# Optimization experiments

Measured on AMD Instinct MI355X. Metric: run time of the kernel, lower is better.

## Reference

```python
import jax, jax.numpy as jnp
import numpy as np

B, I, H = 128, 512, 512


def setup_inputs() -> dict:
    key = jax.random.key(0)
    ks = jax.random.split(key, 6)
    std = float(1.0 / np.sqrt(H))
    return {
        "x": jax.random.normal(ks[0], (B, I), jnp.float32),
        "h_prev": jax.random.normal(ks[1], (B, H), jnp.float32),
        "C_prev": jax.random.normal(ks[2], (B, H, H), jnp.float32),
        "m_prev": jnp.zeros((B, H), jnp.float32),
        "n_prev": jax.random.normal(ks[3], (B, H), jnp.float32),
        "W": jax.random.uniform(ks[4], (6 * H, I), jnp.float32, -std, std),
        "b": jax.random.uniform(ks[5], (6 * H,), jnp.float32, -std, std),
    }


def reference(x, h_prev, C_prev, m_prev, n_prev, W, b):
    # gates: [B, 6H] -> six [B, H] slices (input, forget, output, query, key, value)
    gates = x @ W.T + b
    ig, fg, og, q, k, v = jnp.split(gates, 6, axis=1)
    inv_sqrt_h = jnp.float32(1.0 / np.sqrt(H))
    k_t = inv_sqrt_h * k
    o_t = jax.nn.sigmoid(og)
    # log-domain stabilizer: log(exp(fg)) == fg, log(exp(ig)) == ig
    m_t = jnp.maximum(fg + m_prev, ig)
    i_t = jnp.exp(ig - m_t)
    f_t = jnp.exp(fg + m_prev - m_t)
    # matrix state update: broadcast-add of (i*v*k) column across last dim (as in source)
    C_t = f_t[:, :, None] * C_prev + (i_t * v * k_t)[:, :, None]  # [B,H,H]
    n_t = f_t * n_prev + i_t * k_t  # [B,H]
    # read-out: C_t @ q and n_t . q
    Cq = jnp.einsum("bij,bj->bi", C_t, q)  # [B,H]
    nq = jnp.einsum("bh,bh->b", n_t, q)  # [B]
    denom = jnp.maximum(jnp.abs(nq), jnp.float32(1e-6))
    h_t = o_t * (Cq / denom[:, None])
    return h_t, C_t, m_t, n_t
```

## Files before the change

kernel.cpp:

```cpp
#include <hip/hip_runtime.h>
#include <math.h>


#define B_SZ   128
#define H_DIM  512
#define I_DIM  512
#define G6     3072
#define BH     65536
#define CSZ    33554432

typedef float f32x4 __attribute__((ext_vector_type(4)));

__global__ __launch_bounds__(256) void gemm_gates(
    const float* __restrict__ x, const float* __restrict__ W,
    const float* __restrict__ bias, float* __restrict__ gates) {
  const int tid = threadIdx.x;
  const int c   = (blockIdx.x % 12) * 256 + tid;
  const int b0  = (blockIdx.x / 12) * 4;

  float acc[4];
#pragma unroll
  for (int j = 0; j < 4; ++j) acc[j] = 0.0f;

  const float4* wrow = reinterpret_cast<const float4*>(W + (size_t)c * I_DIM);
  const float4* x4   = reinterpret_cast<const float4*>(x);

#pragma unroll 4
  for (int t4 = 0; t4 < I_DIM / 4; ++t4) {
    const float4 wv = wrow[t4];
#pragma unroll
    for (int j = 0; j < 4; ++j) {
      const float4 xv = x4[(b0 + j) * (I_DIM / 4) + t4];
      acc[j] += xv.x * wv.x + xv.y * wv.y + xv.z * wv.z + xv.w * wv.w;
    }
  }
  const float bi = bias[c];
#pragma unroll
  for (int j = 0; j < 4; ++j)
    gates[(size_t)(b0 + j) * G6 + c] = acc[j] + bi;
}

__global__ __launch_bounds__(512) void gate_pointwise(
    const float* __restrict__ gates, const float* __restrict__ m_prev,
    const float* __restrict__ n_prev, float* __restrict__ out,
    float* __restrict__ f_arr, float* __restrict__ add_arr,
    float* __restrict__ o_arr, float* __restrict__ invden) {
  const int b = blockIdx.x;
  const int h = threadIdx.x;
  const float inv_sqrt_h = 0.044194173824159216f;

  const float* g = gates + (size_t)b * G6;
  float* out_m = out + BH + CSZ;
  float* out_n = out_m + BH;

  const float ig = g[h];
  const float fg = g[512 + h];
  const float og = g[1024 + h];
  const float q  = g[1536 + h];
  const float k  = g[2048 + h];
  const float v  = g[2560 + h];

  const int   idx = b * H_DIM + h;
  const float kt  = inv_sqrt_h * k;
  const float ot  = 1.0f / (1.0f + expf(-og));
  const float mp  = m_prev[idx];
  const float npv = n_prev[idx];
  const float mt  = fmaxf(fg + mp, ig);
  const float it  = expf(ig - mt);
  const float ft  = expf(fg + mp - mt);
  const float nt  = ft * npv + it * kt;

  out_m[idx]   = mt;
  out_n[idx]   = nt;
  f_arr[idx]   = ft;
  add_arr[idx] = it * v * kt;
  o_arr[idx]   = ot;

  __shared__ float red[512];
  red[h] = nt * q;
  __syncthreads();
#pragma unroll
  for (int s = 256; s > 0; s >>= 1) {
    if (h < s) red[h] += red[h + s];
    __syncthreads();
  }
  if (h == 0) {
    const float denom = fmaxf(fabsf(red[0]), 1e-6f);
    invden[b] = 1.0f / denom;
  }
}

__global__ __launch_bounds__(256) void update_C(
    const float* __restrict__ C_prev, const float* __restrict__ gates,
    const float* __restrict__ f_arr, const float* __restrict__ add_arr,
    const float* __restrict__ o_arr, const float* __restrict__ invden,
    float* __restrict__ out) {
  const int tid  = threadIdx.x;
  const int lane = tid & 63;
  const int w    = tid >> 6;
  const int r0   = blockIdx.x * 32;
  const int b    = r0 >> 9;

  const float4* q4 = reinterpret_cast<const float4*>(gates + (size_t)b * G6 + 1536);
  const float4 qa = q4[lane];
  const float4 qb = q4[lane + 64];
  const float inv_d = invden[b];

  float fv[8], av[8], hv[8];
#pragma unroll
  for (int it = 0; it < 8; ++it) {
    const int r = r0 + it * 4 + w;
    fv[it] = f_arr[r];
    av[it] = add_arr[r];
    hv[it] = o_arr[r];
  }

#pragma unroll
  for (int it = 0; it < 8; ++it) {
    const int r = r0 + it * 4 + w;
    const float f = fv[it];
    const float a = av[it];

    const f32x4* cp = reinterpret_cast<const f32x4*>(C_prev) + (size_t)r * 128;
    f32x4*       ct = reinterpret_cast<f32x4*>((float*)out + BH) + (size_t)r * 128;

    const f32x4 c0 = __builtin_nontemporal_load(cp + lane);
    const f32x4 c1 = __builtin_nontemporal_load(cp + lane + 64);

    f32x4 o0, o1;
    o0.x = f * c0.x + a;  o0.y = f * c0.y + a;
    o0.z = f * c0.z + a;  o0.w = f * c0.w + a;
    o1.x = f * c1.x + a;  o1.y = f * c1.y + a;
    o1.z = f * c1.z + a;  o1.w = f * c1.w + a;

    __builtin_nontemporal_store(o0, ct + lane);
    __builtin_nontemporal_store(o1, ct + lane + 64);

    float cq = o0.x * qa.x + o0.y * qa.y + o0.z * qa.z + o0.w * qa.w
             + o1.x * qb.x + o1.y * qb.y + o1.z * qb.z + o1.w * qb.w;
#pragma unroll
    for (int off = 32; off > 0; off >>= 1)
      cq += __shfl_xor(cq, off, 64);
    if (lane == 0)
      out[r] = hv[it] * cq * inv_d;
  }
}

extern "C" void kernel_launch(void* const* d_in, const int* in_sizes, int n_in,
                              void* d_out, int out_size, void* d_ws, size_t ws_size,
                              hipStream_t stream) {
  const float* x      = (const float*)d_in[0];
  const float* C_prev = (const float*)d_in[2];
  const float* m_prev = (const float*)d_in[3];
  const float* n_prev = (const float*)d_in[4];
  const float* W      = (const float*)d_in[5];
  const float* bias   = (const float*)d_in[6];

  float* out = (float*)d_out;
  float* ws  = (float*)d_ws;

  float* gates   = ws;
  float* f_arr   = ws + 393216;
  float* add_arr = f_arr + BH;
  float* o_arr   = add_arr + BH;
  float* invden  = o_arr + BH;

  gemm_gates<<<384, 256, 0, stream>>>(x, W, bias, gates);
  gate_pointwise<<<B_SZ, 512, 0, stream>>>(gates, m_prev, n_prev, out,
                                           f_arr, add_arr, o_arr, invden);
  update_C<<<BH / 32, 256, 0, stream>>>(C_prev, gates, f_arr, add_arr, o_arr,
                                        invden, out);
}
```

Baseline: 275.8 us.

## Recompute gate scalars in update_C and remap GEMM blocks across XCDs

The per-row forget factor, additive term and output sigmoid are now recomputed inside update_C from the gate buffer and m_prev, instead of being written to and read back from workspace arrays by gate_pointwise. This removes three intermediate arrays and their global traffic, at the cost of some duplicated exp work per row. The gate GEMM now runs as 768 blocks of 128 threads, with block indices remapped so each XCD handles a contiguous group of column tiles, aiming for better L2 reuse of W rows.

```diff
diff --git a/kernel.cpp b/kernel.cpp
--- a/kernel.cpp
+++ b/kernel.cpp
@@ -11,16 +11,21 @@
 
 typedef float f32x4 __attribute__((ext_vector_type(4)));
 
-__global__ __launch_bounds__(256) void gemm_gates(
+__global__ __launch_bounds__(128) void gemm_gates(
     const float* __restrict__ x, const float* __restrict__ W,
     const float* __restrict__ bias, float* __restrict__ gates) {
-  const int tid = threadIdx.x;
-  const int c   = (blockIdx.x % 12) * 256 + tid;
-  const int b0  = (blockIdx.x / 12) * 4;
+  const int tid   = threadIdx.x;
+  const int blk   = blockIdx.x;
+  const int xcd   = blk & 7;
+  const int j     = blk >> 3;
+  const int ctile = xcd * 3 + (j % 3);
+  const int btile = j / 3;
+  const int c     = ctile * 128 + tid;
+  const int b0    = btile * 4;
 
   float acc[4];
 #pragma unroll
-  for (int j = 0; j < 4; ++j) acc[j] = 0.0f;
+  for (int jj = 0; jj < 4; ++jj) acc[jj] = 0.0f;
 
   const float4* wrow = reinterpret_cast<const float4*>(W + (size_t)c * I_DIM);
   const float4* x4   = reinterpret_cast<const float4*>(x);
@@ -29,22 +34,21 @@
   for (int t4 = 0; t4 < I_DIM / 4; ++t4) {
     const float4 wv = wrow[t4];
 #pragma unroll
-    for (int j = 0; j < 4; ++j) {
-      const float4 xv = x4[(b0 + j) * (I_DIM / 4) + t4];
-      acc[j] += xv.x * wv.x + xv.y * wv.y + xv.z * wv.z + xv.w * wv.w;
+    for (int jj = 0; jj < 4; ++jj) {
+      const float4 xv = x4[(b0 + jj) * (I_DIM / 4) + t4];
+      acc[jj] += xv.x * wv.x + xv.y * wv.y + xv.z * wv.z + xv.w * wv.w;
     }
   }
   const float bi = bias[c];
 #pragma unroll
-  for (int j = 0; j < 4; ++j)
-    gates[(size_t)(b0 + j) * G6 + c] = acc[j] + bi;
+  for (int jj = 0; jj < 4; ++jj)
+    gates[(size_t)(b0 + jj) * G6 + c] = acc[jj] + bi;
 }
 
 __global__ __launch_bounds__(512) void gate_pointwise(
     const float* __restrict__ gates, const float* __restrict__ m_prev,
     const float* __restrict__ n_prev, float* __restrict__ out,
-    float* __restrict__ f_arr, float* __restrict__ add_arr,
-    float* __restrict__ o_arr, float* __restrict__ invden) {
+    float* __restrict__ invden) {
   const int b = blockIdx.x;
   const int h = threadIdx.x;
   const float inv_sqrt_h = 0.044194173824159216f;
@@ -55,14 +59,11 @@
 
   const float ig = g[h];
   const float fg = g[512 + h];
-  const float og = g[1024 + h];
   const float q  = g[1536 + h];
   const float k  = g[2048 + h];
-  const float v  = g[2560 + h];
 
   const int   idx = b * H_DIM + h;
   const float kt  = inv_sqrt_h * k;
-  const float ot  = 1.0f / (1.0f + expf(-og));
   const float mp  = m_prev[idx];
   const float npv = n_prev[idx];
   const float mt  = fmaxf(fg + mp, ig);
@@ -70,11 +71,8 @@
   const float ft  = expf(fg + mp - mt);
   const float nt  = ft * npv + it * kt;
 
-  out_m[idx]   = mt;
-  out_n[idx]   = nt;
-  f_arr[idx]   = ft;
-  add_arr[idx] = it * v * kt;
-  o_arr[idx]   = ot;
+  out_m[idx] = mt;
+  out_n[idx] = nt;
 
   __shared__ float red[512];
   red[h] = nt * q;
@@ -92,16 +90,18 @@
 
 __global__ __launch_bounds__(256) void update_C(
     const float* __restrict__ C_prev, const float* __restrict__ gates,
-    const float* __restrict__ f_arr, const float* __restrict__ add_arr,
-    const float* __restrict__ o_arr, const float* __restrict__ invden,
+    const float* __restrict__ m_prev, const float* __restrict__ invden,
     float* __restrict__ out) {
   const int tid  = threadIdx.x;
   const int lane = tid & 63;
   const int w    = tid >> 6;
   const int r0   = blockIdx.x * 32;
   const int b    = r0 >> 9;
+  const int i0   = r0 & 511;
+  const float inv_sqrt_h = 0.044194173824159216f;
 
-  const float4* q4 = reinterpret_cast<const float4*>(gates + (size_t)b * G6 + 1536);
+  const float* g = gates + (size_t)b * G6;
+  const float4* q4 = reinterpret_cast<const float4*>(g + 1536);
   const float4 qa = q4[lane];
   const float4 qb = q4[lane + 64];
   const float inv_d = invden[b];
@@ -109,10 +109,19 @@
   float fv[8], av[8], hv[8];
 #pragma unroll
   for (int it = 0; it < 8; ++it) {
-    const int r = r0 + it * 4 + w;
-    fv[it] = f_arr[r];
-    av[it] = add_arr[r];
-    hv[it] = o_arr[r];
+    const int i  = i0 + it * 4 + w;
+    const float ig = g[i];
+    const float fg = g[512 + i];
+    const float og = g[1024 + i];
+    const float k  = g[2048 + i];
+    const float v  = g[2560 + i];
+    const float mp = m_prev[r0 + it * 4 + w];
+    const float kt = inv_sqrt_h * k;
+    const float mt = fmaxf(fg + mp, ig);
+    const float iv = expf(ig - mt);
+    fv[it] = expf(fg + mp - mt);
+    av[it] = iv * v * kt;
+    hv[it] = 1.0f / (1.0f + expf(-og));
   }
 
 #pragma unroll
@@ -159,15 +168,10 @@
   float* out = (float*)d_out;
   float* ws  = (float*)d_ws;
 
-  float* gates   = ws;
-  float* f_arr   = ws + 393216;
-  float* add_arr = f_arr + BH;
-  float* o_arr   = add_arr + BH;
-  float* invden  = o_arr + BH;
+  float* gates  = ws;
+  float* invden = ws + 393216;
 
-  gemm_gates<<<384, 256, 0, stream>>>(x, W, bias, gates);
-  gate_pointwise<<<B_SZ, 512, 0, stream>>>(gates, m_prev, n_prev, out,
-                                           f_arr, add_arr, o_arr, invden);
-  update_C<<<BH / 32, 256, 0, stream>>>(C_prev, gates, f_arr, add_arr, o_arr,
-                                        invden, out);
+  gemm_gates<<<768, 128, 0, stream>>>(x, W, bias, gates);
+  gate_pointwise<<<B_SZ, 512, 0, stream>>>(gates, m_prev, n_prev, out, invden);
+  update_C<<<BH / 32, 256, 0, stream>>>(C_prev, gates, m_prev, invden, out);
 }
```

New measurement: 274.2 us. No clear change (-0.6%).
